# Performance work log

Hardware: AMD Instinct MI355X
Metric: run time of the kernel (lower is better)

## Reference

```python
import jax, jax.numpy as jnp
import numpy as np
from jax import lax

B, T, D, L, H, F = 2, 128, 256, 8, 4, 2048  # batch, time, dim, max_chunk_len, nhead, dim_feedforward
THRESH = 0.5


def setup_inputs() -> dict:
    key = jax.random.key(0)
    ks = jax.random.split(key, 12)
    s = 0.02
    nrm = lambda k, sh, sc=s: jax.random.normal(k, sh, jnp.float32) * sc
    return {
        "frames": jax.random.normal(ks[0], (B, T, D), jnp.float32),
        "cls_token": jax.random.normal(ks[1], (D,), jnp.float32),
        "Wq": nrm(ks[2], (D, D)), "bq": jnp.zeros((D,), jnp.float32),
        "Wk": nrm(ks[3], (D, D)), "bk": jnp.zeros((D,), jnp.float32),
        "Wv": nrm(ks[4], (D, D)), "bv": jnp.zeros((D,), jnp.float32),
        "Wo": nrm(ks[5], (D, D)), "bo": jnp.zeros((D,), jnp.float32),
        "ln1_g": jnp.ones((D,), jnp.float32), "ln1_b": jnp.zeros((D,), jnp.float32),
        "ln2_g": jnp.ones((D,), jnp.float32), "ln2_b": jnp.zeros((D,), jnp.float32),
        "W1": nrm(ks[6], (D, F)), "b1f": jnp.zeros((F,), jnp.float32),
        "W2": nrm(ks[7], (F, D)), "b2f": jnp.zeros((D,), jnp.float32),
        "We1": nrm(ks[8], (D, D)), "be1": jnp.zeros((D,), jnp.float32),
        "We2": jax.random.normal(ks[9], (D,), jnp.float32) * 0.1,
        "be2": jnp.zeros((), jnp.float32),
    }


def reference(frames, cls_token, Wq, bq, Wk, bk, Wv, bv, Wo, bo,
              ln1_g, ln1_b, ln2_g, ln2_b, W1, b1f, W2, b2f,
              We1, be1, We2, be2):
    """Dynamic chunker: for each start index i, grow window 1..L over frames[i:],
    run a pre-norm TransformerEncoderLayer on [CLS, window], stop at first
    p_eoc > THRESH (or window cap). Emits CLS encodings per chunk.
    Returns (chunks [B,T,D] zero-padded, counts [B])."""
    Bq, Tq, Dq = frames.shape
    dh = Dq // H
    scale = 1.0 / np.sqrt(dh).astype(np.float32)

    def ln(x, g, b):
        m = jnp.mean(x, -1, keepdims=True)
        v = jnp.var(x, -1, keepdims=True)
        return (x - m) * lax.rsqrt(v + 1e-5) * g + b

    def enc_cls(seq, kp):
        # seq: (1+L, D); kp: (1+L,) True = padded key. norm_first encoder layer.
        S = seq.shape[0]
        h = ln(seq, ln1_g, ln1_b)
        q = (h @ Wq + bq).reshape(S, H, dh)
        k = (h @ Wk + bk).reshape(S, H, dh)
        v = (h @ Wv + bv).reshape(S, H, dh)
        scores = jnp.einsum('qhd,khd->hqk', q, k) * scale
        scores = jnp.where(kp[None, None, :], -1e30, scores)
        a = jax.nn.softmax(scores, axis=-1)
        o = jnp.einsum('hqk,khd->qhd', a, v).reshape(S, Dq)
        x = seq + o @ Wo + bo
        h2 = ln(x, ln2_g, ln2_b)
        x = x + jax.nn.relu(h2 @ W1 + b1f) @ W2 + b2f
        return x[0]  # CLS position

    pos = jnp.arange(L)
    ls = jnp.arange(1, L + 1)

    def run(fpad):  # fpad: (T+L, D), one sample
        def step(i, _):
            win = lax.dynamic_slice(fpad, (i, 0), (L, Dq))           # frames[i:i+L] (zero-padded past T)
            seq = jnp.concatenate([cls_token[None, :], win], 0)     # (1+L, D)
            base_pad = (i + pos) >= Tq                               # positions past end of sequence
            kp = jnp.concatenate(
                [jnp.zeros((L, 1), bool),
                 (pos[None, :] >= ls[:, None]) | base_pad[None, :]], 1)  # (L, 1+L) one mask per candidate len
            enc = jax.vmap(enc_cls, in_axes=(None, 0))(seq, kp)      # (L, D) candidate CLS encodings
            p = jax.nn.sigmoid(jax.nn.relu(enc @ We1 + be1) @ We2 + be2)  # (L,) eoc probs
            lmax = jnp.clip(Tq - i, 1, L)
            stop = (p > THRESH) & (ls <= lmax)
            lstar = jnp.where(stop.any(), jnp.argmax(stop) + 1, lmax)
            active = i < Tq
            chunk = jnp.where(active, enc[lstar - 1], jnp.zeros((Dq,), seq.dtype))
            i_new = jnp.where(active, i + lstar.astype(i.dtype), i)
            return i_new, (chunk, active)

        _, (chunks, act) = lax.scan(step, jnp.int32(0), None, length=Tq)
        return chunks, act

    fpadded = jnp.pad(frames, ((0, 0), (0, L), (0, 0)))
    chunks, act = jax.vmap(run)(fpadded)
    counts = act.sum(-1).astype(jnp.int32)
    return chunks, counts
```

## Files before the change

kernel.cpp:

```cpp
#include <hip/hip_runtime.h>

#define DEV __device__ __forceinline__

constexpr int Bc = 2, Tc = 128, Dc = 256, Lc = 8, Hc = 4, DH = 64, Fc = 2048;
constexpr float EPS = 1e-5f, SCALE = 0.125f;
constexpr int NROWS = Bc * Tc * Lc;
constexpr int SLAB = NROWS * Dc;

constexpr int OFF_K     = 0;
constexpr int OFF_VWOH  = OFF_K + Bc * Tc * Dc;
constexpr int OFF_QCLS  = OFF_VWOH + Bc * Tc * Hc * Dc;
constexpr int OFF_KCLS  = OFF_QCLS + Dc;
constexpr int OFF_VWOHC = OFF_KCLS + Dc;
constexpr int OFF_ENC   = OFF_VWOHC + Hc * Dc;
constexpr int OFF_Z     = OFF_ENC + SLAB;

DEV int imin(int a, int b) { return a < b ? a : b; }

DEV float blockReduceSum(float v, float* red) {
#pragma unroll
  for (int off = 32; off; off >>= 1) v += __shfl_down(v, off, 64);
  const int lane = threadIdx.x & 63;
  const int w = threadIdx.x >> 6;
  __syncthreads();
  if (lane == 0) red[w] = v;
  __syncthreads();
  return red[0] + red[1] + red[2] + red[3];
}

__global__ __launch_bounds__(256) void k_prep(
    const float* __restrict__ frames, const float* __restrict__ cls,
    const float* __restrict__ Wq, const float* __restrict__ bq,
    const float* __restrict__ Wk, const float* __restrict__ bk,
    const float* __restrict__ Wv, const float* __restrict__ bv,
    const float* __restrict__ Wo,
    const float* __restrict__ g1, const float* __restrict__ b1,
    float* __restrict__ ws) {
  __shared__ float hsm[Dc];
  __shared__ float vsm[Dc];
  __shared__ float red[4];
  const int d = threadIdx.x;
  const int r = blockIdx.x;

  const float x = (r < Bc * Tc) ? frames[r * Dc + d] : cls[d];
  const float s = blockReduceSum(x, red);
  const float m = s * (1.0f / Dc);
  const float c = x - m;
  const float var = blockReduceSum(c * c, red) * (1.0f / Dc);
  hsm[d] = c * (1.0f / sqrtf(var + EPS)) * g1[d] + b1[d];
  __syncthreads();

  float ka = bk[d], va = bv[d];
  for (int c2 = 0; c2 < Dc; ++c2) {
    const float h = hsm[c2];
    ka = fmaf(h, Wk[c2 * Dc + d], ka);
    va = fmaf(h, Wv[c2 * Dc + d], va);
  }
  if (r < Bc * Tc) ws[OFF_K + r * Dc + d] = ka;
  else             ws[OFF_KCLS + d] = ka;
  vsm[d] = va;
  __syncthreads();

#pragma unroll
  for (int hh = 0; hh < Hc; ++hh) {
    float acc = 0.f;
    for (int c2 = 0; c2 < DH; ++c2)
      acc = fmaf(vsm[hh * DH + c2], Wo[(hh * DH + c2) * Dc + d], acc);
    if (r < Bc * Tc) ws[OFF_VWOH + r * (Hc * Dc) + hh * Dc + d] = acc;
    else             ws[OFF_VWOHC + hh * Dc + d] = acc;
  }
  if (r == Bc * Tc) {
    float qa = bq[d];
    for (int c2 = 0; c2 < Dc; ++c2) qa = fmaf(hsm[c2], Wq[c2 * Dc + d], qa);
    ws[OFF_QCLS + d] = qa;
  }
}

__global__ __launch_bounds__(512) void k_fused(
    const float* __restrict__ cls, const float* __restrict__ bo,
    const float* __restrict__ g2, const float* __restrict__ b2,
    const float* __restrict__ W1, const float* __restrict__ b1f,
    const float* __restrict__ W2, const float* __restrict__ b2f,
    const float* __restrict__ We1, const float* __restrict__ be1,
    const float* __restrict__ We2, const float* __restrict__ be2,
    float* __restrict__ ws) {
  const int wg = blockIdx.x;
  const int i = wg & (Tc - 1);
  const int tid = threadIdx.x;
  const int wv = tid >> 6, lane = tid & 63;
  const int lmax = imin(Tc - i, Lc);

  __shared__ float ts[8][1024];
  __shared__ float h2s[8][256];
  __shared__ float x0s[8][256];
  __shared__ float encs[8][256];
  __shared__ float sv[Hc][Lc + 1];
  __shared__ float aP[Lc][Hc][Lc + 1];
  __shared__ __align__(16) float redA[Lc][4];
  __shared__ __align__(16) float redB[Lc][4];
  __shared__ float zred[8][4];

  if (tid < 256) {
    const int hh = tid >> 6;
    const float qv = ws[OFF_QCLS + hh * DH + lane];
    for (int j = 0; j <= Lc; ++j) {
      float p = 0.f;
      if (j == 0) p = qv * ws[OFF_KCLS + hh * DH + lane];
      else if (j - 1 < lmax) p = qv * ws[OFF_K + (wg + j - 1) * Dc + hh * DH + lane];
#pragma unroll
      for (int off = 32; off; off >>= 1) p += __shfl_down(p, off, 64);
      if (lane == 0) sv[hh][j] = p * SCALE;
    }
  }
  __syncthreads();

  if (tid < Lc * Hc) {
    const int l = (tid >> 2) + 1, h4 = tid & 3;
    if (l <= lmax) {
      float mx = -1e30f;
      for (int j = 0; j <= l; ++j) mx = fmaxf(mx, sv[h4][j]);
      float den = 0.f;
      for (int j = 0; j <= l; ++j) den += expf(sv[h4][j] - mx);
      const float inv = 1.f / den;
      for (int j = 0; j <= l; ++j) aP[l - 1][h4][j] = expf(sv[h4][j] - mx) * inv;
    }
  }
  __syncthreads();

  float x0v[Lc];
  if (tid < 256) {
    const int d = tid;
    const float base = cls[d] + bo[d];
#pragma unroll
    for (int l = 0; l < Lc; ++l) x0v[l] = base;
    for (int j = 0; j <= lmax; ++j) {
      const float* vwp = (j == 0) ? (ws + OFF_VWOHC)
                                  : (ws + OFF_VWOH + (wg + j - 1) * (Hc * Dc));
      for (int h4 = 0; h4 < Hc; ++h4) {
        const float w = vwp[h4 * Dc + d];
        const int lstart = (j == 0) ? 1 : j;
        for (int l = lstart; l <= lmax; ++l) x0v[l - 1] = fmaf(aP[l - 1][h4][j], w, x0v[l - 1]);
      }
    }
#pragma unroll
    for (int l = 0; l < Lc; ++l) {
      float p = x0v[l];
#pragma unroll
      for (int off = 32; off; off >>= 1) p += __shfl_down(p, off, 64);
      if (lane == 0) redA[l][tid >> 6] = p;
    }
  }
  __syncthreads();

  float mean[Lc];
  if (tid < 256) {
#pragma unroll
    for (int l = 0; l < Lc; ++l) {
      const float4 s4 = *(const float4*)redA[l];
      mean[l] = (s4.x + s4.y + s4.z + s4.w) * (1.f / Dc);
    }
#pragma unroll
    for (int l = 0; l < Lc; ++l) {
      const float cv = x0v[l] - mean[l];
      float p = cv * cv;
#pragma unroll
      for (int off = 32; off; off >>= 1) p += __shfl_down(p, off, 64);
      if (lane == 0) redB[l][tid >> 6] = p;
    }
  }
  __syncthreads();

  if (tid < 256) {
    const int d = tid;
    const float g2d = g2[d], b2d = b2[d];
    for (int l = 1; l <= lmax; ++l) {
      const float4 s4 = *(const float4*)redB[l - 1];
      const float var = (s4.x + s4.y + s4.z + s4.w) * (1.f / Dc);
      const float rstd = 1.f / sqrtf(var + EPS);
      h2s[l - 1][d] = (x0v[l - 1] - mean[l - 1]) * rstd * g2d + b2d;
      x0s[l - 1][d] = x0v[l - 1];
    }
    for (int l = lmax + 1; l <= Lc; ++l) {
      h2s[l - 1][d] = 0.f;
      x0s[l - 1][d] = 0.f;
    }
  }
  __syncthreads();

  float u[8][4];
#pragma unroll
  for (int r = 0; r < 8; ++r) { u[r][0] = 0.f; u[r][1] = 0.f; u[r][2] = 0.f; u[r][3] = 0.f; }

  for (int half = 0; half < 2; ++half) {
    const int fg = half * 1024 + tid * 2;
    float t[8][2];
    {
      const float2 bb = *(const float2*)&b1f[fg];
#pragma unroll
      for (int r = 0; r < 8; ++r) { t[r][0] = bb.x; t[r][1] = bb.y; }
    }
    for (int c = 0; c < Dc; c += 4) {
      float2 wv1[4];
#pragma unroll
      for (int k = 0; k < 4; ++k) wv1[k] = *(const float2*)&W1[(c + k) * Fc + fg];
#pragma unroll
      for (int r = 0; r < 8; ++r) {
        const float4 h = *(const float4*)&h2s[r][c];
        const float hv[4] = {h.x, h.y, h.z, h.w};
#pragma unroll
        for (int k = 0; k < 4; ++k) {
          t[r][0] = fmaf(hv[k], wv1[k].x, t[r][0]);
          t[r][1] = fmaf(hv[k], wv1[k].y, t[r][1]);
        }
      }
    }
    __syncthreads();
#pragma unroll
    for (int r = 0; r < 8; ++r) {
      float2 v; v.x = fmaxf(t[r][0], 0.f); v.y = fmaxf(t[r][1], 0.f);
      *(float2*)&ts[r][tid * 2] = v;
    }
    __syncthreads();

    for (int kk = 0; kk < 128; kk += 4) {
      const int kl = wv * 128 + kk;
      const int kg = half * 1024 + kl;
      float4 wv2[4];
#pragma unroll
      for (int k = 0; k < 4; ++k)
        wv2[k] = *(const float4*)&W2[(kg + k) * Dc + lane * 4];
#pragma unroll
      for (int r = 0; r < 8; ++r) {
        const float4 h = *(const float4*)&ts[r][kl];
        const float hv[4] = {h.x, h.y, h.z, h.w};
#pragma unroll
        for (int k = 0; k < 4; ++k) {
          u[r][0] = fmaf(hv[k], wv2[k].x, u[r][0]);
          u[r][1] = fmaf(hv[k], wv2[k].y, u[r][1]);
          u[r][2] = fmaf(hv[k], wv2[k].z, u[r][2]);
          u[r][3] = fmaf(hv[k], wv2[k].w, u[r][3]);
        }
      }
    }
    __syncthreads();
  }

  float* redb = &ts[0][0];
  if (wv < 4) {
#pragma unroll
    for (int r = 0; r < 8; ++r) {
      float4 v; v.x = u[r][0]; v.y = u[r][1]; v.z = u[r][2]; v.w = u[r][3];
      *(float4*)&redb[(wv * 8 + r) * 256 + lane * 4] = v;
    }
  }
  __syncthreads();
  if (wv >= 4) {
#pragma unroll
    for (int r = 0; r < 8; ++r) {
      float4 p = *(float4*)&redb[((wv - 4) * 8 + r) * 256 + lane * 4];
      p.x += u[r][0]; p.y += u[r][1]; p.z += u[r][2]; p.w += u[r][3];
      *(float4*)&redb[((wv - 4) * 8 + r) * 256 + lane * 4] = p;
    }
  }
  __syncthreads();

  {
    const int r = wv, d4 = lane * 4;
    float4 s = *(const float4*)&redb[(0 * 8 + r) * 256 + d4];
    const float4 s1 = *(const float4*)&redb[(1 * 8 + r) * 256 + d4];
    const float4 s2 = *(const float4*)&redb[(2 * 8 + r) * 256 + d4];
    const float4 s3 = *(const float4*)&redb[(3 * 8 + r) * 256 + d4];
    s.x = ((s.x + s1.x) + s2.x) + s3.x;
    s.y = ((s.y + s1.y) + s2.y) + s3.y;
    s.z = ((s.z + s1.z) + s2.z) + s3.z;
    s.w = ((s.w + s1.w) + s2.w) + s3.w;
    const float4 x0 = *(const float4*)&x0s[r][d4];
    const float4 bb = *(const float4*)&b2f[d4];
    float4 e;
    e.x = (x0.x + s.x) + bb.x; e.y = (x0.y + s.y) + bb.y;
    e.z = (x0.z + s.z) + bb.z; e.w = (x0.w + s.w) + bb.w;
    *(float4*)&ws[OFF_ENC + (wg * 8 + r) * Dc + d4] = e;
    *(float4*)&encs[r][d4] = e;
  }
  __syncthreads();

  {
    const int f = tid & 255;
    const int rh = tid >> 8;
    float g[4];
    const float be1f = be1[f];
#pragma unroll
    for (int rr = 0; rr < 4; ++rr) g[rr] = be1f;
    for (int c = 0; c < Dc; ++c) {
      const float w = We1[c * Dc + f];
#pragma unroll
      for (int rr = 0; rr < 4; ++rr) g[rr] = fmaf(encs[rh * 4 + rr][c], w, g[rr]);
    }
    const float w2 = We2[f];
#pragma unroll
    for (int rr = 0; rr < 4; ++rr) {
      float p = fmaxf(g[rr], 0.f) * w2;
#pragma unroll
      for (int off = 32; off; off >>= 1) p += __shfl_down(p, off, 64);
      if (lane == 0) zred[wv][rr] = p;
    }
  }
  __syncthreads();
  if (tid < 8) {
    const int r = tid;
    const int wb = (r < 4) ? 0 : 4;
    const int rl = r & 3;
    const float z = ((zred[wb + 0][rl] + zred[wb + 1][rl]) + zred[wb + 2][rl]) +
                    zred[wb + 3][rl];
    ws[OFF_Z + wg * 8 + r] = z + be2[0];
  }
}

__global__ __launch_bounds__(256) void k_emit(float* __restrict__ ws, float* __restrict__ out) {
  const int b = blockIdx.x;
  const int tid = threadIdx.x;
  __shared__ int lst[Tc];
  __shared__ int path[Tc];
  __shared__ int cnt_s;
  if (tid < Tc) {
    const int i = tid;
    const int lmax = imin(Tc - i, Lc);
    const float* z = ws + OFF_Z + (b * Tc + i) * Lc;
    int ls = lmax;
    for (int l = 1; l <= lmax; ++l) {
      if (z[l - 1] > 0.f) { ls = l; break; }
    }
    lst[tid] = ls;
  }
  __syncthreads();
  if (tid < 64) {
    const int a0 = lst[tid], a1 = lst[64 + tid];
    int cur = 0, s = 0;
    while (cur < Tc) {
      const int l = (cur < 64) ? __shfl(a0, cur, 64) : __shfl(a1, cur - 64, 64);
      if (tid == 0) path[s] = cur * Lc + l - 1;
      ++s;
      cur += l;
    }
    if (tid == 0) cnt_s = s;
  }
  __syncthreads();
  const int c = cnt_s;
  for (int s0 = 0; s0 < Tc; s0 += 8) {
    float v[8];
#pragma unroll
    for (int k = 0; k < 8; ++k) {
      const int s = s0 + k;
      v[k] = (s < c) ? ws[OFF_ENC + (b * Tc * Lc + path[s]) * Dc + tid] : 0.f;
    }
#pragma unroll
    for (int k = 0; k < 8; ++k) out[(b * Tc + s0 + k) * Dc + tid] = v[k];
  }
  if (tid == 0) out[Bc * Tc * Dc + b] = (float)c;
}

extern "C" void kernel_launch(void* const* d_in, const int* in_sizes, int n_in,
                              void* d_out, int out_size, void* d_ws, size_t ws_size,
                              hipStream_t stream) {
  const float* frames = (const float*)d_in[0];
  const float* cls    = (const float*)d_in[1];
  const float* Wq     = (const float*)d_in[2];
  const float* bq     = (const float*)d_in[3];
  const float* Wk     = (const float*)d_in[4];
  const float* bk     = (const float*)d_in[5];
  const float* Wv     = (const float*)d_in[6];
  const float* bv     = (const float*)d_in[7];
  const float* Wo     = (const float*)d_in[8];
  const float* bo     = (const float*)d_in[9];
  const float* g1     = (const float*)d_in[10];
  const float* b1     = (const float*)d_in[11];
  const float* g2     = (const float*)d_in[12];
  const float* b2     = (const float*)d_in[13];
  const float* W1     = (const float*)d_in[14];
  const float* b1f    = (const float*)d_in[15];
  const float* W2     = (const float*)d_in[16];
  const float* b2f    = (const float*)d_in[17];
  const float* We1    = (const float*)d_in[18];
  const float* be1    = (const float*)d_in[19];
  const float* We2    = (const float*)d_in[20];
  const float* be2    = (const float*)d_in[21];
  float* ws = (float*)d_ws;
  float* out = (float*)d_out;

  k_prep<<<Bc * Tc + 1, 256, 0, stream>>>(frames, cls, Wq, bq, Wk, bk, Wv, bv, Wo, g1, b1, ws);
  k_fused<<<Bc * Tc, 512, 0, stream>>>(cls, bo, g2, b2, W1, b1f, W2, b2f, We1, be1, We2, be2, ws);
  k_emit<<<Bc, 256, 0, stream>>>(ws, out);
}
```

Before: 243.4 us.

## Split fused FFN kernel across two blocks per window and move eoc head to separate kernel

The 512-thread fused kernel is replaced by a 256-thread kernel launched twice per window, each block handling one half of the 2048-wide feed-forward dimension. Partial FFN outputs and the residual input go to workspace, and a new kernel sums them, runs the end-of-chunk head and computes the stop length per start index. This doubles the block count for more CU parallelism and adds register double-buffering of W1/W2 loads. In exchange the attention and layernorm prologue is recomputed in both halves, and there is extra global traffic plus one more kernel launch.

```diff
diff --git a/kernel.cpp b/kernel.cpp
--- a/kernel.cpp
+++ b/kernel.cpp
@@ -12,8 +12,11 @@
 constexpr int OFF_QCLS  = OFF_VWOH + Bc * Tc * Hc * Dc;
 constexpr int OFF_KCLS  = OFF_QCLS + Dc;
 constexpr int OFF_VWOHC = OFF_KCLS + Dc;
-constexpr int OFF_ENC   = OFF_VWOHC + Hc * Dc;
-constexpr int OFF_Z     = OFF_ENC + SLAB;
+constexpr int OFF_X0    = OFF_VWOHC + Hc * Dc;
+constexpr int OFF_ENC   = OFF_X0;
+constexpr int OFF_UP    = OFF_X0 + SLAB;
+constexpr int OFF_Z     = OFF_UP + 2 * SLAB;
+constexpr int OFF_LST   = OFF_Z + NROWS;
 
 DEV int imin(int a, int b) { return a < b ? a : b; }
 
@@ -76,15 +79,13 @@
   }
 }
 
-__global__ __launch_bounds__(512) void k_fused(
+__global__ __launch_bounds__(256, 2) void k_half(
     const float* __restrict__ cls, const float* __restrict__ bo,
     const float* __restrict__ g2, const float* __restrict__ b2,
     const float* __restrict__ W1, const float* __restrict__ b1f,
-    const float* __restrict__ W2, const float* __restrict__ b2f,
-    const float* __restrict__ We1, const float* __restrict__ be1,
-    const float* __restrict__ We2, const float* __restrict__ be2,
-    float* __restrict__ ws) {
-  const int wg = blockIdx.x;
+    const float* __restrict__ W2, float* __restrict__ ws) {
+  const int wg = blockIdx.x >> 1;
+  const int half = blockIdx.x & 1;
   const int i = wg & (Tc - 1);
   const int tid = threadIdx.x;
   const int wv = tid >> 6, lane = tid & 63;
@@ -92,24 +93,20 @@
 
   __shared__ float ts[8][1024];
   __shared__ float h2s[8][256];
-  __shared__ float x0s[8][256];
-  __shared__ float encs[8][256];
   __shared__ float sv[Hc][Lc + 1];
   __shared__ float aP[Lc][Hc][Lc + 1];
   __shared__ __align__(16) float redA[Lc][4];
   __shared__ __align__(16) float redB[Lc][4];
-  __shared__ float zred[8][4];
-
-  if (tid < 256) {
-    const int hh = tid >> 6;
-    const float qv = ws[OFF_QCLS + hh * DH + lane];
+
+  {
+    const float qv = ws[OFF_QCLS + wv * DH + lane];
     for (int j = 0; j <= Lc; ++j) {
       float p = 0.f;
-      if (j == 0) p = qv * ws[OFF_KCLS + hh * DH + lane];
-      else if (j - 1 < lmax) p = qv * ws[OFF_K + (wg + j - 1) * Dc + hh * DH + lane];
+      if (j == 0) p = qv * ws[OFF_KCLS + wv * DH + lane];
+      else if (j - 1 < lmax) p = qv * ws[OFF_K + (wg + j - 1) * Dc + wv * DH + lane];
 #pragma unroll
       for (int off = 32; off; off >>= 1) p += __shfl_down(p, off, 64);
-      if (lane == 0) sv[hh][j] = p * SCALE;
+      if (lane == 0) sv[wv][j] = p * SCALE;
     }
   }
   __syncthreads();
@@ -127,9 +124,9 @@
   }
   __syncthreads();
 
+  const int d = tid;
   float x0v[Lc];
-  if (tid < 256) {
-    const int d = tid;
+  {
     const float base = cls[d] + bo[d];
 #pragma unroll
     for (int l = 0; l < Lc; ++l) x0v[l] = base;
@@ -142,177 +139,192 @@
         for (int l = lstart; l <= lmax; ++l) x0v[l - 1] = fmaf(aP[l - 1][h4][j], w, x0v[l - 1]);
       }
     }
-#pragma unroll
-    for (int l = 0; l < Lc; ++l) {
-      float p = x0v[l];
-#pragma unroll
-      for (int off = 32; off; off >>= 1) p += __shfl_down(p, off, 64);
-      if (lane == 0) redA[l][tid >> 6] = p;
-    }
-  }
-  __syncthreads();
-
+  }
+#pragma unroll
+  for (int l = 0; l < Lc; ++l) {
+    float p = x0v[l];
+#pragma unroll
+    for (int off = 32; off; off >>= 1) p += __shfl_down(p, off, 64);
+    if (lane == 0) redA[l][wv] = p;
+  }
+  __syncthreads();
   float mean[Lc];
-  if (tid < 256) {
-#pragma unroll
-    for (int l = 0; l < Lc; ++l) {
-      const float4 s4 = *(const float4*)redA[l];
-      mean[l] = (s4.x + s4.y + s4.z + s4.w) * (1.f / Dc);
-    }
-#pragma unroll
-    for (int l = 0; l < Lc; ++l) {
-      const float cv = x0v[l] - mean[l];
-      float p = cv * cv;
-#pragma unroll
-      for (int off = 32; off; off >>= 1) p += __shfl_down(p, off, 64);
-      if (lane == 0) redB[l][tid >> 6] = p;
-    }
-  }
-  __syncthreads();
-
-  if (tid < 256) {
-    const int d = tid;
+#pragma unroll
+  for (int l = 0; l < Lc; ++l) {
+    const float4 s4 = *(const float4*)redA[l];
+    mean[l] = (s4.x + s4.y + s4.z + s4.w) * (1.f / Dc);
+  }
+#pragma unroll
+  for (int l = 0; l < Lc; ++l) {
+    const float cv = x0v[l] - mean[l];
+    float p = cv * cv;
+#pragma unroll
+    for (int off = 32; off; off >>= 1) p += __shfl_down(p, off, 64);
+    if (lane == 0) redB[l][wv] = p;
+  }
+  __syncthreads();
+
+  {
     const float g2d = g2[d], b2d = b2[d];
     for (int l = 1; l <= lmax; ++l) {
       const float4 s4 = *(const float4*)redB[l - 1];
       const float var = (s4.x + s4.y + s4.z + s4.w) * (1.f / Dc);
       const float rstd = 1.f / sqrtf(var + EPS);
       h2s[l - 1][d] = (x0v[l - 1] - mean[l - 1]) * rstd * g2d + b2d;
-      x0s[l - 1][d] = x0v[l - 1];
+      if (half == 0) ws[OFF_X0 + (wg * Lc + l - 1) * Dc + d] = x0v[l - 1];
     }
     for (int l = lmax + 1; l <= Lc; ++l) {
       h2s[l - 1][d] = 0.f;
-      x0s[l - 1][d] = 0.f;
-    }
-  }
-  __syncthreads();
-
-  float u[8][4];
-#pragma unroll
-  for (int r = 0; r < 8; ++r) { u[r][0] = 0.f; u[r][1] = 0.f; u[r][2] = 0.f; u[r][3] = 0.f; }
-
-  for (int half = 0; half < 2; ++half) {
-    const int fg = half * 1024 + tid * 2;
-    float t[8][2];
-    {
-      const float2 bb = *(const float2*)&b1f[fg];
-#pragma unroll
-      for (int r = 0; r < 8; ++r) { t[r][0] = bb.x; t[r][1] = bb.y; }
-    }
+      if (half == 0) ws[OFF_X0 + (wg * Lc + l - 1) * Dc + d] = 0.f;
+    }
+  }
+  __syncthreads();
+
+  const int fg = half * 1024 + tid * 4;
+  float t[8][4];
+  {
+    const float4 bb = *(const float4*)&b1f[fg];
+#pragma unroll
+    for (int r = 0; r < 8; ++r) { t[r][0] = bb.x; t[r][1] = bb.y; t[r][2] = bb.z; t[r][3] = bb.w; }
+  }
+  {
+    float4 cur[4];
+#pragma unroll
+    for (int k = 0; k < 4; ++k) cur[k] = *(const float4*)&W1[k * Fc + fg];
     for (int c = 0; c < Dc; c += 4) {
-      float2 wv1[4];
-#pragma unroll
-      for (int k = 0; k < 4; ++k) wv1[k] = *(const float2*)&W1[(c + k) * Fc + fg];
+      float4 nxt[4];
+      const int cn = (c + 4 < Dc) ? c + 4 : 0;
+#pragma unroll
+      for (int k = 0; k < 4; ++k) nxt[k] = *(const float4*)&W1[(cn + k) * Fc + fg];
 #pragma unroll
       for (int r = 0; r < 8; ++r) {
         const float4 h = *(const float4*)&h2s[r][c];
         const float hv[4] = {h.x, h.y, h.z, h.w};
 #pragma unroll
         for (int k = 0; k < 4; ++k) {
-          t[r][0] = fmaf(hv[k], wv1[k].x, t[r][0]);
-          t[r][1] = fmaf(hv[k], wv1[k].y, t[r][1]);
+          t[r][0] = fmaf(hv[k], cur[k].x, t[r][0]);
+          t[r][1] = fmaf(hv[k], cur[k].y, t[r][1]);
+          t[r][2] = fmaf(hv[k], cur[k].z, t[r][2]);
+          t[r][3] = fmaf(hv[k], cur[k].w, t[r][3]);
         }
       }
-    }
-    __syncthreads();
-#pragma unroll
-    for (int r = 0; r < 8; ++r) {
-      float2 v; v.x = fmaxf(t[r][0], 0.f); v.y = fmaxf(t[r][1], 0.f);
-      *(float2*)&ts[r][tid * 2] = v;
-    }
-    __syncthreads();
-
-    for (int kk = 0; kk < 128; kk += 4) {
-      const int kl = wv * 128 + kk;
-      const int kg = half * 1024 + kl;
-      float4 wv2[4];
-#pragma unroll
-      for (int k = 0; k < 4; ++k)
-        wv2[k] = *(const float4*)&W2[(kg + k) * Dc + lane * 4];
+#pragma unroll
+      for (int k = 0; k < 4; ++k) cur[k] = nxt[k];
+    }
+  }
+#pragma unroll
+  for (int r = 0; r < 8; ++r) {
+    float4 v;
+    v.x = fmaxf(t[r][0], 0.f); v.y = fmaxf(t[r][1], 0.f);
+    v.z = fmaxf(t[r][2], 0.f); v.w = fmaxf(t[r][3], 0.f);
+    *(float4*)&ts[r][tid * 4] = v;
+  }
+  __syncthreads();
+
+  const int d4 = lane * 4;
+  const int kbase = half * 1024 + wv * 256;
+  float u[8][4];
+#pragma unroll
+  for (int r = 0; r < 8; ++r) { u[r][0] = 0.f; u[r][1] = 0.f; u[r][2] = 0.f; u[r][3] = 0.f; }
+  {
+    float4 cur[4];
+#pragma unroll
+    for (int k = 0; k < 4; ++k) cur[k] = *(const float4*)&W2[(kbase + k) * Dc + d4];
+    for (int kk = 0; kk < 256; kk += 4) {
+      float4 nxt[4];
+      const int kn = (kk + 4 < 256) ? kk + 4 : 0;
+#pragma unroll
+      for (int k = 0; k < 4; ++k) nxt[k] = *(const float4*)&W2[(kbase + kn + k) * Dc + d4];
 #pragma unroll
       for (int r = 0; r < 8; ++r) {
-        const float4 h = *(const float4*)&ts[r][kl];
+        const float4 h = *(const float4*)&ts[r][wv * 256 + kk];
         const float hv[4] = {h.x, h.y, h.z, h.w};
 #pragma unroll
         for (int k = 0; k < 4; ++k) {
-          u[r][0] = fmaf(hv[k], wv2[k].x, u[r][0]);
-          u[r][1] = fmaf(hv[k], wv2[k].y, u[r][1]);
-          u[r][2] = fmaf(hv[k], wv2[k].z, u[r][2]);
-          u[r][3] = fmaf(hv[k], wv2[k].w, u[r][3]);
+          u[r][0] = fmaf(hv[k], cur[k].x, u[r][0]);
+          u[r][1] = fmaf(hv[k], cur[k].y, u[r][1]);
+          u[r][2] = fmaf(hv[k], cur[k].z, u[r][2]);
+          u[r][3] = fmaf(hv[k], cur[k].w, u[r][3]);
         }
       }
-    }
-    __syncthreads();
-  }
+#pragma unroll
+      for (int k = 0; k < 4; ++k) cur[k] = nxt[k];
+    }
+  }
+  __syncthreads();
 
   float* redb = &ts[0][0];
-  if (wv < 4) {
+#pragma unroll
+  for (int r = 0; r < 8; ++r) {
+    float4 v; v.x = u[r][0]; v.y = u[r][1]; v.z = u[r][2]; v.w = u[r][3];
+    *(float4*)&redb[(wv * 8 + r) * 256 + d4] = v;
+  }
+  __syncthreads();
+  {
+    float* up = ws + OFF_UP + half * SLAB;
 #pragma unroll
     for (int r = 0; r < 8; ++r) {
-      float4 v; v.x = u[r][0]; v.y = u[r][1]; v.z = u[r][2]; v.w = u[r][3];
-      *(float4*)&redb[(wv * 8 + r) * 256 + lane * 4] = v;
-    }
-  }
-  __syncthreads();
-  if (wv >= 4) {
-#pragma unroll
-    for (int r = 0; r < 8; ++r) {
-      float4 p = *(float4*)&redb[((wv - 4) * 8 + r) * 256 + lane * 4];
-      p.x += u[r][0]; p.y += u[r][1]; p.z += u[r][2]; p.w += u[r][3];
-      *(float4*)&redb[((wv - 4) * 8 + r) * 256 + lane * 4] = p;
-    }
-  }
-  __syncthreads();
-
-  {
-    const int r = wv, d4 = lane * 4;
-    float4 s = *(const float4*)&redb[(0 * 8 + r) * 256 + d4];
-    const float4 s1 = *(const float4*)&redb[(1 * 8 + r) * 256 + d4];
-    const float4 s2 = *(const float4*)&redb[(2 * 8 + r) * 256 + d4];
-    const float4 s3 = *(const float4*)&redb[(3 * 8 + r) * 256 + d4];
-    s.x = ((s.x + s1.x) + s2.x) + s3.x;
-    s.y = ((s.y + s1.y) + s2.y) + s3.y;
-    s.z = ((s.z + s1.z) + s2.z) + s3.z;
-    s.w = ((s.w + s1.w) + s2.w) + s3.w;
-    const float4 x0 = *(const float4*)&x0s[r][d4];
-    const float4 bb = *(const float4*)&b2f[d4];
-    float4 e;
-    e.x = (x0.x + s.x) + bb.x; e.y = (x0.y + s.y) + bb.y;
-    e.z = (x0.z + s.z) + bb.z; e.w = (x0.w + s.w) + bb.w;
-    *(float4*)&ws[OFF_ENC + (wg * 8 + r) * Dc + d4] = e;
-    *(float4*)&encs[r][d4] = e;
-  }
-  __syncthreads();
-
-  {
-    const int f = tid & 255;
-    const int rh = tid >> 8;
-    float g[4];
-    const float be1f = be1[f];
-#pragma unroll
-    for (int rr = 0; rr < 4; ++rr) g[rr] = be1f;
-    for (int c = 0; c < Dc; ++c) {
-      const float w = We1[c * Dc + f];
-#pragma unroll
-      for (int rr = 0; rr < 4; ++rr) g[rr] = fmaf(encs[rh * 4 + rr][c], w, g[rr]);
-    }
-    const float w2 = We2[f];
-#pragma unroll
-    for (int rr = 0; rr < 4; ++rr) {
-      float p = fmaxf(g[rr], 0.f) * w2;
-#pragma unroll
-      for (int off = 32; off; off >>= 1) p += __shfl_down(p, off, 64);
-      if (lane == 0) zred[wv][rr] = p;
-    }
-  }
-  __syncthreads();
-  if (tid < 8) {
-    const int r = tid;
-    const int wb = (r < 4) ? 0 : 4;
-    const int rl = r & 3;
-    const float z = ((zred[wb + 0][rl] + zred[wb + 1][rl]) + zred[wb + 2][rl]) +
-                    zred[wb + 3][rl];
-    ws[OFF_Z + wg * 8 + r] = z + be2[0];
+      const float s = ((redb[(0 * 8 + r) * 256 + tid] + redb[(1 * 8 + r) * 256 + tid]) +
+                       redb[(2 * 8 + r) * 256 + tid]) + redb[(3 * 8 + r) * 256 + tid];
+      up[(wg * Lc + r) * Dc + tid] = s;
+    }
+  }
+}
+
+__global__ __launch_bounds__(256) void k_encz(
+    const float* __restrict__ We1, const float* __restrict__ be1,
+    const float* __restrict__ We2, const float* __restrict__ be2,
+    const float* __restrict__ b2f, float* __restrict__ ws) {
+  const int wg = blockIdx.x;
+  const int f = threadIdx.x;
+  const int lane = f & 63, wv = f >> 6;
+  __shared__ float encs[8][Dc];
+  __shared__ __align__(16) float zred[8][4];
+  __shared__ float zs[8];
+  const float bb = b2f[f];
+#pragma unroll
+  for (int r = 0; r < 8; ++r) {
+    const int row = wg * Lc + r;
+    const float e = ws[OFF_X0 + row * Dc + f] +
+                    ws[OFF_UP + row * Dc + f] +
+                    ws[OFF_UP + SLAB + row * Dc + f] + bb;
+    ws[OFF_ENC + row * Dc + f] = e;
+    encs[r][f] = e;
+  }
+  __syncthreads();
+
+  float g[8];
+  const float be1f = be1[f];
+#pragma unroll
+  for (int r = 0; r < 8; ++r) g[r] = be1f;
+  for (int c = 0; c < Dc; ++c) {
+    const float w = We1[c * Dc + f];
+#pragma unroll
+    for (int r = 0; r < 8; ++r) g[r] = fmaf(encs[r][c], w, g[r]);
+  }
+  const float w2 = We2[f];
+#pragma unroll
+  for (int r = 0; r < 8; ++r) {
+    float p = fmaxf(g[r], 0.f) * w2;
+#pragma unroll
+    for (int off = 32; off; off >>= 1) p += __shfl_down(p, off, 64);
+    if (lane == 0) zred[r][wv] = p;
+  }
+  __syncthreads();
+  if (f < 8) {
+    const float4 s4 = *(const float4*)zred[f];
+    zs[f] = s4.x + s4.y + s4.z + s4.w + be2[0];
+    ws[OFF_Z + wg * Lc + f] = zs[f];
+  }
+  __syncthreads();
+  if (f == 0) {
+    const int i = wg & (Tc - 1);
+    const int lmax = imin(Tc - i, Lc);
+    int ls = lmax;
+    for (int l = 1; l <= lmax; ++l) {
+      if (zs[l - 1] > 0.f) { ls = l; break; }
+    }
+    ((int*)(ws + OFF_LST))[wg] = ls;
   }
 }
 
@@ -322,16 +334,8 @@
   __shared__ int lst[Tc];
   __shared__ int path[Tc];
   __shared__ int cnt_s;
-  if (tid < Tc) {
-    const int i = tid;
-    const int lmax = imin(Tc - i, Lc);
-    const float* z = ws + OFF_Z + (b * Tc + i) * Lc;
-    int ls = lmax;
-    for (int l = 1; l <= lmax; ++l) {
-      if (z[l - 1] > 0.f) { ls = l; break; }
-    }
-    lst[tid] = ls;
-  }
+  const int* lsrc = (const int*)(ws + OFF_LST);
+  if (tid < Tc) lst[tid] = lsrc[b * Tc + tid];
   __syncthreads();
   if (tid < 64) {
     const int a0 = lst[tid], a1 = lst[64 + tid];
@@ -388,6 +392,7 @@
   float* out = (float*)d_out;
 
   k_prep<<<Bc * Tc + 1, 256, 0, stream>>>(frames, cls, Wq, bq, Wk, bk, Wv, bv, Wo, g1, b1, ws);
-  k_fused<<<Bc * Tc, 512, 0, stream>>>(cls, bo, g2, b2, W1, b1f, W2, b2f, We1, be1, We2, be2, ws);
+  k_half<<<2 * Bc * Tc, 256, 0, stream>>>(cls, bo, g2, b2, W1, b1f, W2, ws);
+  k_encz<<<Bc * Tc, 256, 0, stream>>>(We1, be1, We2, be2, b2f, ws);
   k_emit<<<Bc, 256, 0, stream>>>(ws, out);
 }
```

Result: slower. 299.0 us (+22.8%).

## Compute full FFN hidden in one pass with float4 W1 loads and 8-way reduction

Applied to the files above, without the earlier changes.

The FFN first layer now computes all 2048 hidden units in a single pass, each thread doing 4 columns with float4 W1 loads, instead of two halves of 2 columns each. The full 8x2048 ReLU activation tile goes into shared memory (doubling ts to 64KB), removing two barriers per half. The second GEMM gives each wave 256 K-rows, and the partial sums are reduced 8-way through shared memory in one step rather than pairwise. The larger shared footprint and more live registers (t[8][4] plus u) may lower occupancy.

```diff
diff --git a/kernel.cpp b/kernel.cpp
--- a/kernel.cpp
+++ b/kernel.cpp
@@ -90,10 +90,10 @@
   const int wv = tid >> 6, lane = tid & 63;
   const int lmax = imin(Tc - i, Lc);
 
-  __shared__ float ts[8][1024];
-  __shared__ float h2s[8][256];
-  __shared__ float x0s[8][256];
-  __shared__ float encs[8][256];
+  __shared__ __align__(16) float ts[8][2048];
+  __shared__ __align__(16) float h2s[8][256];
+  __shared__ __align__(16) float x0s[8][256];
+  __shared__ __align__(16) float encs[8][256];
   __shared__ float sv[Hc][Lc + 1];
   __shared__ float aP[Lc][Hc][Lc + 1];
   __shared__ __align__(16) float redA[Lc][4];
@@ -187,100 +187,87 @@
   }
   __syncthreads();
 
+  const int fg = tid * 4;
+  float t[8][4];
+  {
+    const float4 bb = *(const float4*)&b1f[fg];
+#pragma unroll
+    for (int r = 0; r < 8; ++r) { t[r][0] = bb.x; t[r][1] = bb.y; t[r][2] = bb.z; t[r][3] = bb.w; }
+  }
+  for (int c = 0; c < Dc; c += 4) {
+    float4 w1v[4];
+#pragma unroll
+    for (int k = 0; k < 4; ++k) w1v[k] = *(const float4*)&W1[(c + k) * Fc + fg];
+#pragma unroll
+    for (int r = 0; r < 8; ++r) {
+      const float4 h = *(const float4*)&h2s[r][c];
+      const float hv[4] = {h.x, h.y, h.z, h.w};
+#pragma unroll
+      for (int k = 0; k < 4; ++k) {
+        t[r][0] = fmaf(hv[k], w1v[k].x, t[r][0]);
+        t[r][1] = fmaf(hv[k], w1v[k].y, t[r][1]);
+        t[r][2] = fmaf(hv[k], w1v[k].z, t[r][2]);
+        t[r][3] = fmaf(hv[k], w1v[k].w, t[r][3]);
+      }
+    }
+  }
+#pragma unroll
+  for (int r = 0; r < 8; ++r) {
+    float4 v;
+    v.x = fmaxf(t[r][0], 0.f); v.y = fmaxf(t[r][1], 0.f);
+    v.z = fmaxf(t[r][2], 0.f); v.w = fmaxf(t[r][3], 0.f);
+    *(float4*)&ts[r][fg] = v;
+  }
+  __syncthreads();
+
+  const int d4 = lane * 4;
   float u[8][4];
 #pragma unroll
   for (int r = 0; r < 8; ++r) { u[r][0] = 0.f; u[r][1] = 0.f; u[r][2] = 0.f; u[r][3] = 0.f; }
-
-  for (int half = 0; half < 2; ++half) {
-    const int fg = half * 1024 + tid * 2;
-    float t[8][2];
-    {
-      const float2 bb = *(const float2*)&b1f[fg];
-#pragma unroll
-      for (int r = 0; r < 8; ++r) { t[r][0] = bb.x; t[r][1] = bb.y; }
-    }
-    for (int c = 0; c < Dc; c += 4) {
-      float2 wv1[4];
-#pragma unroll
-      for (int k = 0; k < 4; ++k) wv1[k] = *(const float2*)&W1[(c + k) * Fc + fg];
-#pragma unroll
-      for (int r = 0; r < 8; ++r) {
-        const float4 h = *(const float4*)&h2s[r][c];
-        const float hv[4] = {h.x, h.y, h.z, h.w};
-#pragma unroll
-        for (int k = 0; k < 4; ++k) {
-          t[r][0] = fmaf(hv[k], wv1[k].x, t[r][0]);
-          t[r][1] = fmaf(hv[k], wv1[k].y, t[r][1]);
-        }
+  for (int kk = 0; kk < 256; kk += 4) {
+    const int kg = wv * 256 + kk;
+    float4 w2v[4];
+#pragma unroll
+    for (int k = 0; k < 4; ++k) w2v[k] = *(const float4*)&W2[(kg + k) * Dc + d4];
+#pragma unroll
+    for (int r = 0; r < 8; ++r) {
+      const float4 h = *(const float4*)&ts[r][kg];
+      const float hv[4] = {h.x, h.y, h.z, h.w};
+#pragma unroll
+      for (int k = 0; k < 4; ++k) {
+        u[r][0] = fmaf(hv[k], w2v[k].x, u[r][0]);
+        u[r][1] = fmaf(hv[k], w2v[k].y, u[r][1]);
+        u[r][2] = fmaf(hv[k], w2v[k].z, u[r][2]);
+        u[r][3] = fmaf(hv[k], w2v[k].w, u[r][3]);
       }
     }
-    __syncthreads();
-#pragma unroll
-    for (int r = 0; r < 8; ++r) {
-      float2 v; v.x = fmaxf(t[r][0], 0.f); v.y = fmaxf(t[r][1], 0.f);
-      *(float2*)&ts[r][tid * 2] = v;
-    }
-    __syncthreads();
-
-    for (int kk = 0; kk < 128; kk += 4) {
-      const int kl = wv * 128 + kk;
-      const int kg = half * 1024 + kl;
-      float4 wv2[4];
-#pragma unroll
-      for (int k = 0; k < 4; ++k)
-        wv2[k] = *(const float4*)&W2[(kg + k) * Dc + lane * 4];
-#pragma unroll
-      for (int r = 0; r < 8; ++r) {
-        const float4 h = *(const float4*)&ts[r][kl];
-        const float hv[4] = {h.x, h.y, h.z, h.w};
-#pragma unroll
-        for (int k = 0; k < 4; ++k) {
-          u[r][0] = fmaf(hv[k], wv2[k].x, u[r][0]);
-          u[r][1] = fmaf(hv[k], wv2[k].y, u[r][1]);
-          u[r][2] = fmaf(hv[k], wv2[k].z, u[r][2]);
-          u[r][3] = fmaf(hv[k], wv2[k].w, u[r][3]);
-        }
-      }
-    }
-    __syncthreads();
-  }
+  }
+  __syncthreads();
 
   float* redb = &ts[0][0];
-  if (wv < 4) {
-#pragma unroll
-    for (int r = 0; r < 8; ++r) {
-      float4 v; v.x = u[r][0]; v.y = u[r][1]; v.z = u[r][2]; v.w = u[r][3];
-      *(float4*)&redb[(wv * 8 + r) * 256 + lane * 4] = v;
-    }
-  }
-  __syncthreads();
-  if (wv >= 4) {
-#pragma unroll
-    for (int r = 0; r < 8; ++r) {
-      float4 p = *(float4*)&redb[((wv - 4) * 8 + r) * 256 + lane * 4];
-      p.x += u[r][0]; p.y += u[r][1]; p.z += u[r][2]; p.w += u[r][3];
-      *(float4*)&redb[((wv - 4) * 8 + r) * 256 + lane * 4] = p;
-    }
+#pragma unroll
+  for (int r = 0; r < 8; ++r) {
+    float4 v; v.x = u[r][0]; v.y = u[r][1]; v.z = u[r][2]; v.w = u[r][3];
+    *(float4*)&redb[(wv * 8 + r) * 256 + d4] = v;
   }
   __syncthreads();
 
   {
-    const int r = wv, d4 = lane * 4;
-    float4 s = *(const float4*)&redb[(0 * 8 + r) * 256 + d4];
-    const float4 s1 = *(const float4*)&redb[(1 * 8 + r) * 256 + d4];
-    const float4 s2 = *(const float4*)&redb[(2 * 8 + r) * 256 + d4];
-    const float4 s3 = *(const float4*)&redb[(3 * 8 + r) * 256 + d4];
-    s.x = ((s.x + s1.x) + s2.x) + s3.x;
-    s.y = ((s.y + s1.y) + s2.y) + s3.y;
-    s.z = ((s.z + s1.z) + s2.z) + s3.z;
-    s.w = ((s.w + s1.w) + s2.w) + s3.w;
-    const float4 x0 = *(const float4*)&x0s[r][d4];
-    const float4 bb = *(const float4*)&b2f[d4];
+    const int r = tid >> 6;
+    const int dg = (tid & 63) * 4;
+    float4 s = *(const float4*)&redb[(0 * 8 + r) * 256 + dg];
+#pragma unroll
+    for (int w = 1; w < 8; ++w) {
+      const float4 p = *(const float4*)&redb[(w * 8 + r) * 256 + dg];
+      s.x += p.x; s.y += p.y; s.z += p.z; s.w += p.w;
+    }
+    const float4 x0 = *(const float4*)&x0s[r][dg];
+    const float4 bb = *(const float4*)&b2f[dg];
     float4 e;
     e.x = (x0.x + s.x) + bb.x; e.y = (x0.y + s.y) + bb.y;
     e.z = (x0.z + s.z) + bb.z; e.w = (x0.w + s.w) + bb.w;
-    *(float4*)&ws[OFF_ENC + (wg * 8 + r) * Dc + d4] = e;
-    *(float4*)&encs[r][d4] = e;
+    *(float4*)&ws[OFF_ENC + (wg * 8 + r) * Dc + dg] = e;
+    *(float4*)&encs[r][dg] = e;
   }
   __syncthreads();
 
```

Result: faster. 231.2 us (-5.0%).
